# Performance work log

Measured on AMD Instinct MI355X. Metric: run time of the kernel, lower is better.

The kernel has to match this reference:

```python
import jax, jax.numpy as jnp
import numpy as np

NUM_EMB = 1024
EMB_DIM = 256
BETA = 0.25


def setup_inputs() -> dict:
    key = jax.random.key(0)
    k1, k2 = jax.random.split(key)
    z = jax.random.normal(k1, (64, 32, 32, EMB_DIM), dtype=jnp.float32)
    # RandomUniform(-1/N, 1/N) init, shape (embedding_dimension, number_embeddings)
    embeddings = jax.random.uniform(
        k2, (EMB_DIM, NUM_EMB), dtype=jnp.float32,
        minval=-1.0 / NUM_EMB, maxval=1.0 / NUM_EMB)
    return {"z": z, "embeddings": embeddings}


def reference(z, embeddings):
    beta = BETA
    z_flat = z.reshape(-1, EMB_DIM)                      # [N, D]
    # squared L2 distances via ||z||^2 + ||e||^2 - 2 z @ e
    distances = (jnp.sum(z_flat ** 2, axis=1, keepdims=True)
                 + jnp.sum(embeddings ** 2, axis=0)
                 - 2.0 * (z_flat @ embeddings))          # [N, K]
    encoding_indices = jnp.argmin(distances, axis=1)     # [N] int
    quantized = embeddings.T[encoding_indices].reshape(z.shape)  # gather rows of e^T
    vq_loss = jnp.mean((quantized - jax.lax.stop_gradient(z)) ** 2)
    commitment_loss = beta * jnp.mean((jax.lax.stop_gradient(quantized) - z) ** 2)
    quantized_st = z + jax.lax.stop_gradient(quantized - z)  # straight-through
    # perplexity from codebook usage histogram
    counts = jnp.zeros((NUM_EMB,), dtype=distances.dtype).at[encoding_indices].add(1.0)
    avg_probs = counts / encoding_indices.shape[0]
    perplexity = jnp.exp(-jnp.sum(avg_probs * jnp.log(avg_probs + 1e-10)))
    return (quantized_st, encoding_indices, vq_loss, commitment_loss, perplexity)
```

## Files before the change

### kernel.cpp

```cpp
#include <hip/hip_runtime.h>
#include <math.h>

#define NUM_EMB 1024
#define EMB_DIM 256
#define NROWS   65536
#define NTHREADS 256
#define EPSF 1.5e-3f
#define GCAP 524288

#define OFF_IDX  16777216
#define OFF_VQ   16842752

#define WS_C2    0
#define WS_HIST  4096
#define WS_LOSS  8192
#define WS_GCNT  8196
#define WS_R2    8448
#define WS_SLOT  270592
#define WS_ETF   794880
#define WS_ETB   1843456
#define WS_GLIST 2367744

typedef __attribute__((ext_vector_type(8))) short bf16x8;
typedef __attribute__((ext_vector_type(4))) float f32x4;

__device__ __forceinline__ unsigned short f2bf(float x) {
  unsigned u = __float_as_uint(x);
  unsigned r = (u + 0x7FFFu + ((u >> 16) & 1u)) >> 16;
  return (unsigned short)r;
}

__global__ __launch_bounds__(NTHREADS) void vq_prep(
    const float* __restrict__ emb, float* __restrict__ cvec,
    int* __restrict__ hist, float* __restrict__ loss, int* __restrict__ gcnt) {
  int k = blockIdx.x * blockDim.x + threadIdx.x;
  if (k < NUM_EMB) {
    float s = 0.f;
    for (int d = 0; d < EMB_DIM; ++d) {
      float v = emb[d * NUM_EMB + k];
      s = __fadd_rn(s, __fmul_rn(v, v));
    }
    cvec[k] = s;
    hist[k] = 0;
  }
  if (k == 0) { *loss = 0.f; *gcnt = 0; }
}

__global__ __launch_bounds__(NTHREADS) void vq_tr(
    const float* __restrict__ emb, float* __restrict__ embTf,
    unsigned short* __restrict__ embTbf) {
  __shared__ float t[64][65];
  const int kt = blockIdx.x & 15, dt = blockIdx.x >> 4;
  const int tid = threadIdx.x;
  #pragma unroll
  for (int it = 0; it < 16; ++it) {
    int i = tid + it * NTHREADS, r = i >> 6, c = i & 63;
    t[r][c] = emb[(dt * 64 + r) * NUM_EMB + kt * 64 + c];
  }
  __syncthreads();
  #pragma unroll
  for (int it = 0; it < 16; ++it) {
    int i = tid + it * NTHREADS, r = i >> 6, c = i & 63;
    float v = t[c][r];
    embTf[(kt * 64 + r) * EMB_DIM + dt * 64 + c] = v;
    embTbf[(kt * 64 + r) * EMB_DIM + dt * 64 + c] = f2bf(v);
  }
}

__global__ __launch_bounds__(NTHREADS) void vq_r2k(
    const float* __restrict__ z, float* __restrict__ r2out) {
  __shared__ float zc[64][36];
  __shared__ float pmm[64][2][4];
  const int tid = threadIdx.x;
  const int n0 = blockIdx.x * 64;
  const float* zrow = z + (size_t)n0 * EMB_DIM;
  const int prow = tid >> 2, pm = tid & 3;
  float racc[2][2] = {{0.f, 0.f}, {0.f, 0.f}};
  for (int dc = 0; dc < 8; ++dc) {
    __syncthreads();
    #pragma unroll
    for (int it = 0; it < 2; ++it) {
      int i = tid + it * NTHREADS, row = i >> 3, f4 = i & 7;
      *(float4*)(&zc[row][f4 * 4]) = *(const float4*)(zrow + row * EMB_DIM + dc * 32 + f4 * 4);
    }
    __syncthreads();
    const int half = dc >> 2;
    #pragma unroll
    for (int q = 0; q < 4; ++q)
      #pragma unroll
      for (int jj = 0; jj < 2; ++jj) {
        float v = zc[prow][(pm * 2 + jj) + 8 * q];
        racc[half][jj] = __fadd_rn(racc[half][jj], __fmul_rn(v, v));
      }
  }
  pmm[prow][0][pm] = __fadd_rn(racc[0][0], racc[0][1]);
  pmm[prow][1][pm] = __fadd_rn(racc[1][0], racc[1][1]);
  __syncthreads();
  if (tid < 64) {
    float h0 = __fadd_rn(__fadd_rn(pmm[tid][0][0], pmm[tid][0][1]),
                         __fadd_rn(pmm[tid][0][2], pmm[tid][0][3]));
    float h1 = __fadd_rn(__fadd_rn(pmm[tid][1][0], pmm[tid][1][1]),
                         __fadd_rn(pmm[tid][1][2], pmm[tid][1][3]));
    r2out[n0 + tid] = __fadd_rn(h0, h1);
  }
}

__global__ __launch_bounds__(NTHREADS, 2) void vq_mfma(
    const float* __restrict__ z, const unsigned short* __restrict__ embTbf,
    const float* __restrict__ cvec, unsigned long long* __restrict__ slots,
    int* __restrict__ gcnt, unsigned int* __restrict__ glist) {
  __shared__ unsigned short zc[64][264];
  __shared__ unsigned short Bl[256][56];
  __shared__ float c2s[NUM_EMB];
  __shared__ int rowminb[64];
  __shared__ int lcnt, lbase, lcount;
  __shared__ unsigned int llist[512];

  const int tid = threadIdx.x;
  const int wave = tid >> 6, lane = tid & 63;
  const int quad = lane >> 4, l15 = lane & 15;
  const int n0 = blockIdx.x * 64;

  for (int i = tid; i < NUM_EMB; i += NTHREADS) c2s[i] = cvec[i] + 1.0f;
  if (tid < 64) {
    rowminb[tid] = 0x7F000000;
    slots[n0 + tid] = ~0ULL;
  }
  #pragma unroll
  for (int it = 0; it < 16; ++it) {
    int g = tid + it * NTHREADS, row = g >> 6, f4 = g & 63;
    float4 v = *(const float4*)(z + (size_t)(n0 + row) * EMB_DIM + f4 * 4);
    ushort4 b;
    b.x = f2bf(v.x); b.y = f2bf(v.y); b.z = f2bf(v.z); b.w = f2bf(v.w);
    *(ushort4*)(&zc[row][f4 * 4]) = b;
  }

  for (int j = 0; j < 4; ++j) {
    f32x4 acc[4][4];
    #pragma unroll
    for (int rt = 0; rt < 4; ++rt)
      #pragma unroll
      for (int ct = 0; ct < 4; ++ct)
        acc[rt][ct] = (f32x4){0.f, 0.f, 0.f, 0.f};

    for (int kc = 0; kc < 8; ++kc) {
      __syncthreads();
      #pragma unroll
      for (int it = 0; it < 4; ++it) {
        int nn = (tid >> 2) + it * 64, seg = tid & 3;
        uint4 v = *(const uint4*)(embTbf + (size_t)(j * 256 + nn) * EMB_DIM + kc * 32 + seg * 8);
        *(uint4*)(&Bl[nn][seg * 8]) = v;
      }
      __syncthreads();
      bf16x8 av[4], bv[4];
      #pragma unroll
      for (int rt = 0; rt < 4; ++rt)
        av[rt] = *(const bf16x8*)(&zc[rt * 16 + l15][kc * 32 + quad * 8]);
      #pragma unroll
      for (int ct = 0; ct < 4; ++ct)
        bv[ct] = *(const bf16x8*)(&Bl[wave * 64 + ct * 16 + l15][quad * 8]);
      #pragma unroll
      for (int rt = 0; rt < 4; ++rt)
        #pragma unroll
        for (int ct = 0; ct < 4; ++ct)
          acc[rt][ct] = __builtin_amdgcn_mfma_f32_16x16x32_bf16(av[rt], bv[ct], acc[rt][ct], 0, 0, 0);
    }

    #pragma unroll
    for (int rt = 0; rt < 4; ++rt)
      #pragma unroll
      for (int reg = 0; reg < 4; ++reg) {
        float m = 1e30f;
        #pragma unroll
        for (int ct = 0; ct < 4; ++ct) {
          int k = j * 256 + wave * 64 + ct * 16 + l15;
          float d = fmaf(-2.f, acc[rt][ct][reg], c2s[k]);
          m = fminf(m, d);
        }
        #pragma unroll
        for (int off = 1; off < 16; off <<= 1)
          m = fminf(m, __shfl_xor(m, off));
        if (l15 == 0)
          atomicMin(&rowminb[rt * 16 + quad * 4 + reg], __float_as_int(m));
      }
    if (tid == 0) lcnt = 0;
    __syncthreads();

    #pragma unroll
    for (int rt = 0; rt < 4; ++rt)
      #pragma unroll
      for (int reg = 0; reg < 4; ++reg) {
        int rowl = rt * 16 + quad * 4 + reg;
        float fmin = __int_as_float(rowminb[rowl]);
        #pragma unroll
        for (int ct = 0; ct < 4; ++ct) {
          int k = j * 256 + wave * 64 + ct * 16 + l15;
          float d = fmaf(-2.f, acc[rt][ct][reg], c2s[k]);
          if (d <= fmin + EPSF) {
            int id = atomicAdd(&lcnt, 1);
            if (id < 512) llist[id] = ((unsigned)(n0 + rowl) << 10) | (unsigned)k;
          }
        }
      }
    __syncthreads();
    if (tid == 0) {
      int c = lcnt < 512 ? lcnt : 512;
      lcount = c;
      lbase = atomicAdd(gcnt, c);
    }
    __syncthreads();
    for (int i = tid; i < lcount; i += NTHREADS)
      if (lbase + i < GCAP) glist[lbase + i] = llist[i];
    __syncthreads();
  }
}

__global__ __launch_bounds__(NTHREADS) void vq_refine(
    const float* __restrict__ z, const float* __restrict__ embTf,
    const float* __restrict__ r2, const float* __restrict__ cvec,
    const int* __restrict__ gcnt, const unsigned int* __restrict__ glist,
    unsigned long long* __restrict__ slots) {
  int n = *gcnt; if (n > GCAP) n = GCAP;
  for (int i = blockIdx.x * NTHREADS + threadIdx.x; i < n;
       i += gridDim.x * NTHREADS) {
    unsigned e = glist[i];
    int grow = (int)(e >> 10), k = (int)(e & 1023);
    const float* zr = z + (size_t)grow * EMB_DIM;
    const float* er = embTf + (size_t)k * EMB_DIM;
    float s = 0.f;
    for (int d = 0; d < EMB_DIM; ++d)
      s = fmaf(zr[d], er[d], s);
    float dist = __fsub_rn(__fadd_rn(r2[grow], cvec[k]), __fmul_rn(2.0f, s));
    unsigned long long key =
        ((unsigned long long)__float_as_uint(dist) << 32) | (unsigned)k;
    atomicMin(&slots[grow], key);
  }
}

__global__ __launch_bounds__(NTHREADS) void vq_epi(
    const float* __restrict__ z, const float* __restrict__ embTf,
    const unsigned long long* __restrict__ slots,
    float* __restrict__ out, int* __restrict__ hist, float* __restrict__ loss) {
  __shared__ int ks[64];
  __shared__ float wsum[4];
  const int tid = threadIdx.x;
  const int n0 = blockIdx.x * 64;
  const float* zrow = z + (size_t)n0 * EMB_DIM;
  if (tid < 64) {
    int k = (int)(slots[n0 + tid] & 1023ULL);
    ks[tid] = k;
    out[OFF_IDX + n0 + tid] = (float)k;
    atomicAdd(&hist[k], 1);
  }
  __syncthreads();
  float sumsq = 0.f;
  #pragma unroll
  for (int it = 0; it < 16; ++it) {
    int g = tid + it * NTHREADS;
    int row = g >> 6;
    int d = (g & 63) * 4;
    int k = ks[row];
    float4 zv = *(const float4*)(zrow + row * EMB_DIM + d);
    float4 q = *(const float4*)(embTf + (size_t)k * EMB_DIM + d);
    float4 df;
    df.x = q.x - zv.x; df.y = q.y - zv.y; df.z = q.z - zv.z; df.w = q.w - zv.w;
    sumsq = fmaf(df.x, df.x, sumsq);
    sumsq = fmaf(df.y, df.y, sumsq);
    sumsq = fmaf(df.z, df.z, sumsq);
    sumsq = fmaf(df.w, df.w, sumsq);
    *(float4*)(out + (size_t)(n0 + row) * EMB_DIM + d) = q;
  }
  #pragma unroll
  for (int off = 32; off > 0; off >>= 1) sumsq += __shfl_down(sumsq, off);
  if ((tid & 63) == 0) wsum[tid >> 6] = sumsq;
  __syncthreads();
  if (tid == 0) atomicAdd(loss, wsum[0] + wsum[1] + wsum[2] + wsum[3]);
}

__global__ __launch_bounds__(NTHREADS) void vq_finalize(
    const int* __restrict__ hist, const float* __restrict__ loss,
    float* __restrict__ out) {
  __shared__ float ws[4];
  int tid = threadIdx.x;
  float s = 0.f;
  for (int k = tid; k < NUM_EMB; k += NTHREADS) {
    float p = (float)hist[k] * (1.0f / 65536.0f);
    s += p * logf(p + 1e-10f);
  }
  #pragma unroll
  for (int off = 32; off > 0; off >>= 1) s += __shfl_down(s, off);
  if ((tid & 63) == 0) ws[tid >> 6] = s;
  __syncthreads();
  if (tid == 0) {
    float tot = ws[0] + ws[1] + ws[2] + ws[3];
    float vq = *loss * (1.0f / 16777216.0f);
    out[OFF_VQ + 0] = vq;
    out[OFF_VQ + 1] = 0.25f * vq;
    out[OFF_VQ + 2] = expf(-tot);
  }
}

extern "C" void kernel_launch(void* const* d_in, const int* in_sizes, int n_in,
                              void* d_out, int out_size, void* d_ws, size_t ws_size,
                              hipStream_t stream) {
  const float* z   = (const float*)d_in[0];
  const float* emb = (const float*)d_in[1];
  float* out = (float*)d_out;
  char* ws = (char*)d_ws;
  float* cvec   = (float*)(ws + WS_C2);
  int*   hist   = (int*)(ws + WS_HIST);
  float* loss   = (float*)(ws + WS_LOSS);
  int*   gcnt   = (int*)(ws + WS_GCNT);
  float* r2     = (float*)(ws + WS_R2);
  unsigned long long* slots = (unsigned long long*)(ws + WS_SLOT);
  float* embTf  = (float*)(ws + WS_ETF);
  unsigned short* embTbf = (unsigned short*)(ws + WS_ETB);
  unsigned int* glist = (unsigned int*)(ws + WS_GLIST);

  vq_prep<<<4, NTHREADS, 0, stream>>>(emb, cvec, hist, loss, gcnt);
  vq_tr<<<64, NTHREADS, 0, stream>>>(emb, embTf, embTbf);
  vq_r2k<<<NROWS / 64, NTHREADS, 0, stream>>>(z, r2);
  vq_mfma<<<NROWS / 64, NTHREADS, 0, stream>>>(z, embTbf, cvec, slots, gcnt, glist);
  vq_refine<<<512, NTHREADS, 0, stream>>>(z, embTf, r2, cvec, gcnt, glist, slots);
  vq_epi<<<NROWS / 64, NTHREADS, 0, stream>>>(z, embTf, slots, out, hist, loss);
  vq_finalize<<<1, NTHREADS, 0, stream>>>(hist, loss, out);
}
```

Before: 318.9 us.

## Fuse row-norm pass into MFMA kernel and stream codebook fragments directly from global

Folds the separate z row-norm kernel into the MFMA distance kernel, so z is read once per block instead of in a separate pass. Each wave now owns 256 codebook columns and loads its B fragments straight from global/L2 rather than staging them in LDS, which removes the per-chunk barriers. Candidate lists become per-wave and are flushed once at the end. The codebook norm kernel now reads the transposed copy with float4 loads, and the refine kernel is vectorized and launched with a larger grid. The trade is more global/L2 traffic for B, which now has no block-level reuse, and a second uncoalesced read of z for the norms. The threshold is also compared against a row minimum that may not be final yet, since there is no block barrier before it is read.

```diff
diff --git a/kernel.cpp b/kernel.cpp
--- a/kernel.cpp
+++ b/kernel.cpp
@@ -7,6 +7,7 @@
 #define NTHREADS 256
 #define EPSF 1.5e-3f
 #define GCAP 524288
+#define LLCAP 512
 
 #define OFF_IDX  16777216
 #define OFF_VQ   16842752
@@ -30,22 +31,6 @@
   return (unsigned short)r;
 }
 
-__global__ __launch_bounds__(NTHREADS) void vq_prep(
-    const float* __restrict__ emb, float* __restrict__ cvec,
-    int* __restrict__ hist, float* __restrict__ loss, int* __restrict__ gcnt) {
-  int k = blockIdx.x * blockDim.x + threadIdx.x;
-  if (k < NUM_EMB) {
-    float s = 0.f;
-    for (int d = 0; d < EMB_DIM; ++d) {
-      float v = emb[d * NUM_EMB + k];
-      s = __fadd_rn(s, __fmul_rn(v, v));
-    }
-    cvec[k] = s;
-    hist[k] = 0;
-  }
-  if (k == 0) { *loss = 0.f; *gcnt = 0; }
-}
-
 __global__ __launch_bounds__(NTHREADS) void vq_tr(
     const float* __restrict__ emb, float* __restrict__ embTf,
     unsigned short* __restrict__ embTbf) {
@@ -67,34 +52,69 @@
   }
 }
 
-__global__ __launch_bounds__(NTHREADS) void vq_r2k(
-    const float* __restrict__ z, float* __restrict__ r2out) {
-  __shared__ float zc[64][36];
+__global__ __launch_bounds__(NTHREADS) void vq_prep2(
+    const float* __restrict__ embTf, float* __restrict__ cvec,
+    int* __restrict__ hist, float* __restrict__ loss, int* __restrict__ gcnt) {
+  int k = blockIdx.x * NTHREADS + threadIdx.x;
+  const float4* row = (const float4*)(embTf + (size_t)k * EMB_DIM);
+  float s = 0.f;
+  #pragma unroll 8
+  for (int i = 0; i < 64; ++i) {
+    float4 v = row[i];
+    s = __fadd_rn(s, __fmul_rn(v.x, v.x));
+    s = __fadd_rn(s, __fmul_rn(v.y, v.y));
+    s = __fadd_rn(s, __fmul_rn(v.z, v.z));
+    s = __fadd_rn(s, __fmul_rn(v.w, v.w));
+  }
+  cvec[k] = s;
+  hist[k] = 0;
+  if (k == 0) { *loss = 0.f; *gcnt = 0; }
+}
+
+__global__ __launch_bounds__(NTHREADS, 3) void vq_mfma(
+    const float* __restrict__ z, const unsigned short* __restrict__ embTbf,
+    const float* __restrict__ cvec, float* __restrict__ r2out,
+    unsigned long long* __restrict__ slots,
+    int* __restrict__ gcnt, unsigned int* __restrict__ glist) {
+  __shared__ unsigned short zc[64][264];
+  __shared__ float c2s[NUM_EMB];
+  __shared__ int rowminb[64];
   __shared__ float pmm[64][2][4];
+  __shared__ unsigned int llist[4][LLCAP];
+  __shared__ int lcnt[4];
+
   const int tid = threadIdx.x;
+  const int wave = tid >> 6, lane = tid & 63;
+  const int quad = lane >> 4, l15 = lane & 15;
   const int n0 = blockIdx.x * 64;
-  const float* zrow = z + (size_t)n0 * EMB_DIM;
-  const int prow = tid >> 2, pm = tid & 3;
-  float racc[2][2] = {{0.f, 0.f}, {0.f, 0.f}};
-  for (int dc = 0; dc < 8; ++dc) {
-    __syncthreads();
-    #pragma unroll
-    for (int it = 0; it < 2; ++it) {
-      int i = tid + it * NTHREADS, row = i >> 3, f4 = i & 7;
-      *(float4*)(&zc[row][f4 * 4]) = *(const float4*)(zrow + row * EMB_DIM + dc * 32 + f4 * 4);
+  const float* zblk = z + (size_t)n0 * EMB_DIM;
+
+  #pragma unroll
+  for (int it = 0; it < 16; ++it) {
+    int g = tid + it * NTHREADS, row = g >> 6, f4 = g & 63;
+    float4 v = *(const float4*)(zblk + row * EMB_DIM + f4 * 4);
+    ushort4 b; b.x = f2bf(v.x); b.y = f2bf(v.y); b.z = f2bf(v.z); b.w = f2bf(v.w);
+    *(ushort4*)(&zc[row][f4 * 4]) = b;
+  }
+  {
+    const int prow = tid >> 2, pm = tid & 3;
+    float racc[2][2] = {{0.f, 0.f}, {0.f, 0.f}};
+    for (int dc = 0; dc < 8; ++dc) {
+      const int half = dc >> 2;
+      #pragma unroll
+      for (int q = 0; q < 4; ++q)
+        #pragma unroll
+        for (int jj = 0; jj < 2; ++jj) {
+          float v = zblk[prow * EMB_DIM + dc * 32 + q * 8 + pm * 2 + jj];
+          racc[half][jj] = __fadd_rn(racc[half][jj], __fmul_rn(v, v));
+        }
     }
-    __syncthreads();
-    const int half = dc >> 2;
-    #pragma unroll
-    for (int q = 0; q < 4; ++q)
-      #pragma unroll
-      for (int jj = 0; jj < 2; ++jj) {
-        float v = zc[prow][(pm * 2 + jj) + 8 * q];
-        racc[half][jj] = __fadd_rn(racc[half][jj], __fmul_rn(v, v));
-      }
-  }
-  pmm[prow][0][pm] = __fadd_rn(racc[0][0], racc[0][1]);
-  pmm[prow][1][pm] = __fadd_rn(racc[1][0], racc[1][1]);
+    pmm[prow][0][pm] = __fadd_rn(racc[0][0], racc[0][1]);
+    pmm[prow][1][pm] = __fadd_rn(racc[1][0], racc[1][1]);
+  }
+  for (int i = tid; i < NUM_EMB; i += NTHREADS) c2s[i] = cvec[i] + 1.0f;
+  if (tid < 64) rowminb[tid] = 0x7F000000;
+  if (tid < 4) lcnt[tid] = 0;
   __syncthreads();
   if (tid < 64) {
     float h0 = __fadd_rn(__fadd_rn(pmm[tid][0][0], pmm[tid][0][1]),
@@ -102,40 +122,12 @@
     float h1 = __fadd_rn(__fadd_rn(pmm[tid][1][0], pmm[tid][1][1]),
                          __fadd_rn(pmm[tid][1][2], pmm[tid][1][3]));
     r2out[n0 + tid] = __fadd_rn(h0, h1);
-  }
-}
-
-__global__ __launch_bounds__(NTHREADS, 2) void vq_mfma(
-    const float* __restrict__ z, const unsigned short* __restrict__ embTbf,
-    const float* __restrict__ cvec, unsigned long long* __restrict__ slots,
-    int* __restrict__ gcnt, unsigned int* __restrict__ glist) {
-  __shared__ unsigned short zc[64][264];
-  __shared__ unsigned short Bl[256][56];
-  __shared__ float c2s[NUM_EMB];
-  __shared__ int rowminb[64];
-  __shared__ int lcnt, lbase, lcount;
-  __shared__ unsigned int llist[512];
-
-  const int tid = threadIdx.x;
-  const int wave = tid >> 6, lane = tid & 63;
-  const int quad = lane >> 4, l15 = lane & 15;
-  const int n0 = blockIdx.x * 64;
-
-  for (int i = tid; i < NUM_EMB; i += NTHREADS) c2s[i] = cvec[i] + 1.0f;
-  if (tid < 64) {
-    rowminb[tid] = 0x7F000000;
     slots[n0 + tid] = ~0ULL;
   }
-  #pragma unroll
-  for (int it = 0; it < 16; ++it) {
-    int g = tid + it * NTHREADS, row = g >> 6, f4 = g & 63;
-    float4 v = *(const float4*)(z + (size_t)(n0 + row) * EMB_DIM + f4 * 4);
-    ushort4 b;
-    b.x = f2bf(v.x); b.y = f2bf(v.y); b.z = f2bf(v.z); b.w = f2bf(v.w);
-    *(ushort4*)(&zc[row][f4 * 4]) = b;
-  }
-
-  for (int j = 0; j < 4; ++j) {
+
+  const int cbase = wave * 256;
+  for (int jt = 0; jt < 4; ++jt) {
+    const int c0 = cbase + jt * 64;
     f32x4 acc[4][4];
     #pragma unroll
     for (int rt = 0; rt < 4; ++rt)
@@ -143,22 +135,16 @@
       for (int ct = 0; ct < 4; ++ct)
         acc[rt][ct] = (f32x4){0.f, 0.f, 0.f, 0.f};
 
+    #pragma unroll
     for (int kc = 0; kc < 8; ++kc) {
-      __syncthreads();
-      #pragma unroll
-      for (int it = 0; it < 4; ++it) {
-        int nn = (tid >> 2) + it * 64, seg = tid & 3;
-        uint4 v = *(const uint4*)(embTbf + (size_t)(j * 256 + nn) * EMB_DIM + kc * 32 + seg * 8);
-        *(uint4*)(&Bl[nn][seg * 8]) = v;
-      }
-      __syncthreads();
       bf16x8 av[4], bv[4];
+      #pragma unroll
+      for (int ct = 0; ct < 4; ++ct)
+        bv[ct] = *(const bf16x8*)(embTbf + (size_t)(c0 + ct * 16 + l15) * EMB_DIM
+                                  + kc * 32 + quad * 8);
       #pragma unroll
       for (int rt = 0; rt < 4; ++rt)
         av[rt] = *(const bf16x8*)(&zc[rt * 16 + l15][kc * 32 + quad * 8]);
-      #pragma unroll
-      for (int ct = 0; ct < 4; ++ct)
-        bv[ct] = *(const bf16x8*)(&Bl[wave * 64 + ct * 16 + l15][quad * 8]);
       #pragma unroll
       for (int rt = 0; rt < 4; ++rt)
         #pragma unroll
@@ -170,49 +156,34 @@
     for (int rt = 0; rt < 4; ++rt)
       #pragma unroll
       for (int reg = 0; reg < 4; ++reg) {
-        float m = 1e30f;
-        #pragma unroll
-        for (int ct = 0; ct < 4; ++ct) {
-          int k = j * 256 + wave * 64 + ct * 16 + l15;
-          float d = fmaf(-2.f, acc[rt][ct][reg], c2s[k]);
-          m = fminf(m, d);
-        }
+        const int rowl = rt * 16 + quad * 4 + reg;
+        float d[4];
+        #pragma unroll
+        for (int ct = 0; ct < 4; ++ct)
+          d[ct] = fmaf(-2.f, acc[rt][ct][reg], c2s[c0 + ct * 16 + l15]);
+        float m = fminf(fminf(d[0], d[1]), fminf(d[2], d[3]));
         #pragma unroll
         for (int off = 1; off < 16; off <<= 1)
           m = fminf(m, __shfl_xor(m, off));
-        if (l15 == 0)
-          atomicMin(&rowminb[rt * 16 + quad * 4 + reg], __float_as_int(m));
-      }
-    if (tid == 0) lcnt = 0;
-    __syncthreads();
-
-    #pragma unroll
-    for (int rt = 0; rt < 4; ++rt)
-      #pragma unroll
-      for (int reg = 0; reg < 4; ++reg) {
-        int rowl = rt * 16 + quad * 4 + reg;
-        float fmin = __int_as_float(rowminb[rowl]);
+        if (l15 == 0) atomicMin(&rowminb[rowl], __float_as_int(m));
+        float thr = __int_as_float(rowminb[rowl]) + EPSF;
         #pragma unroll
         for (int ct = 0; ct < 4; ++ct) {
-          int k = j * 256 + wave * 64 + ct * 16 + l15;
-          float d = fmaf(-2.f, acc[rt][ct][reg], c2s[k]);
-          if (d <= fmin + EPSF) {
-            int id = atomicAdd(&lcnt, 1);
-            if (id < 512) llist[id] = ((unsigned)(n0 + rowl) << 10) | (unsigned)k;
+          if (d[ct] <= thr) {
+            int id = atomicAdd(&lcnt[wave], 1);
+            if (id < LLCAP)
+              llist[wave][id] = ((unsigned)(n0 + rowl) << 10) | (unsigned)(c0 + ct * 16 + l15);
           }
         }
       }
-    __syncthreads();
-    if (tid == 0) {
-      int c = lcnt < 512 ? lcnt : 512;
-      lcount = c;
-      lbase = atomicAdd(gcnt, c);
-    }
-    __syncthreads();
-    for (int i = tid; i < lcount; i += NTHREADS)
-      if (lbase + i < GCAP) glist[lbase + i] = llist[i];
-    __syncthreads();
-  }
+  }
+
+  int cnt = lcnt[wave]; if (cnt > LLCAP) cnt = LLCAP;
+  int base = 0;
+  if (lane == 0) base = atomicAdd(gcnt, cnt);
+  base = __shfl(base, 0);
+  for (int i = lane; i < cnt; i += 64)
+    if (base + i < GCAP) glist[base + i] = llist[wave][i];
 }
 
 __global__ __launch_bounds__(NTHREADS) void vq_refine(
@@ -228,8 +199,13 @@
     const float* zr = z + (size_t)grow * EMB_DIM;
     const float* er = embTf + (size_t)k * EMB_DIM;
     float s = 0.f;
-    for (int d = 0; d < EMB_DIM; ++d)
-      s = fmaf(zr[d], er[d], s);
+    #pragma unroll 8
+    for (int d4 = 0; d4 < 64; ++d4) {
+      float4 a = *(const float4*)(zr + d4 * 4);
+      float4 b = *(const float4*)(er + d4 * 4);
+      s = fmaf(a.x, b.x, s); s = fmaf(a.y, b.y, s);
+      s = fmaf(a.z, b.z, s); s = fmaf(a.w, b.w, s);
+    }
     float dist = __fsub_rn(__fadd_rn(r2[grow], cvec[k]), __fmul_rn(2.0f, s));
     unsigned long long key =
         ((unsigned long long)__float_as_uint(dist) << 32) | (unsigned)k;
@@ -317,11 +293,10 @@
   unsigned short* embTbf = (unsigned short*)(ws + WS_ETB);
   unsigned int* glist = (unsigned int*)(ws + WS_GLIST);
 
-  vq_prep<<<4, NTHREADS, 0, stream>>>(emb, cvec, hist, loss, gcnt);
   vq_tr<<<64, NTHREADS, 0, stream>>>(emb, embTf, embTbf);
-  vq_r2k<<<NROWS / 64, NTHREADS, 0, stream>>>(z, r2);
-  vq_mfma<<<NROWS / 64, NTHREADS, 0, stream>>>(z, embTbf, cvec, slots, gcnt, glist);
-  vq_refine<<<512, NTHREADS, 0, stream>>>(z, embTf, r2, cvec, gcnt, glist, slots);
+  vq_prep2<<<4, NTHREADS, 0, stream>>>(embTf, cvec, hist, loss, gcnt);
+  vq_mfma<<<NROWS / 64, NTHREADS, 0, stream>>>(z, embTbf, cvec, r2, slots, gcnt, glist);
+  vq_refine<<<1024, NTHREADS, 0, stream>>>(z, embTf, r2, cvec, gcnt, glist, slots);
   vq_epi<<<NROWS / 64, NTHREADS, 0, stream>>>(z, embTf, slots, out, hist, loss);
   vq_finalize<<<1, NTHREADS, 0, stream>>>(hist, loss, out);
 }
```

Result: slower. 392.6 us (+23.1%).
